# Kernel tuning notes

Hardware: AMD Instinct MI355X
Metric: run time of the kernel (lower is better)

Reference implementation:

```python
import jax, jax.numpy as jnp
import numpy as np
import math

# ---- physical constants (QMAV) ----
MASS = 1.5
GRAV = 9.81
_J_NP = np.diag([0.0211, 0.0219, 0.0366]).astype(np.float32)
J = jnp.asarray(_J_NP)
J_INV = jnp.asarray(np.linalg.inv(_J_NP).astype(np.float32))
KD_X = KD_Y = KD_Z = 0.10   # linear drag coeffs
K_H = 0.01                   # horizontal-velocity lift coeff
O_MIN, O_MAX = 0.0, 1000.0   # rotor speed limits [rad/s]
KT, KM, ARM = 1.0e-5, 1.0e-7, 0.15
_G_VEC = jnp.array([0.0, 0.0, GRAV], jnp.float32).reshape(1, 3, 1)  # NED, down positive


def make_G1():
    # [T, Mx, My, Mz] = G_1 @ [o1^2, o2^2, o3^2, o4^2], X-configuration mixer
    c = ARM * KT * math.sqrt(2.0) / 2.0
    return np.array([
        [KT,  KT,  KT,  KT],
        [-c,   c,   c,  -c],
        [-c,  -c,   c,   c],
        [-KM,  KM, -KM,  KM],
    ], dtype=np.float32)


def quat_to_rot(q):
    # q: [B,4,1] = (ew,ex,ey,ez) -> body-to-inertial rotation [B,3,3]
    ew, ex, ey, ez = q[:, 0, 0], q[:, 1, 0], q[:, 2, 0], q[:, 3, 0]
    r = jnp.stack([
        ew**2 + ex**2 - ey**2 - ez**2, 2*(ex*ey - ew*ez), 2*(ex*ez + ew*ey),
        2*(ex*ey + ew*ez), ew**2 - ex**2 + ey**2 - ez**2, 2*(ey*ez - ew*ex),
        2*(ex*ez - ew*ey), 2*(ey*ez + ew*ex), ew**2 - ex**2 - ey**2 + ez**2,
    ], axis=-1)
    return r.reshape(-1, 3, 3)


def quat_to_euler(q):
    ew, ex, ey, ez = q[:, 0:1, :], q[:, 1:2, :], q[:, 2:3, :], q[:, 3:4, :]
    phi = jnp.arctan2(2*(ew*ex + ey*ez), ew**2 + ez**2 - ex**2 - ey**2)
    theta = jnp.arcsin(jnp.clip(2*(ew*ey - ex*ez), -1.0, 1.0))
    psi = jnp.arctan2(2*(ew*ez + ex*ey), ew**2 + ex**2 - ey**2 - ez**2)
    return phi, theta, psi


def rigid_body_deriv(x, u):
    # x: [B,13,1] = [pos(3), v_world(3), quat(4), omega(3)]; u: [B,6,1] = [f_inertial(3), moment_body(3)]
    v = x[:, 3:6, :]
    q = x[:, 6:10, :]
    w = x[:, 10:13, :]
    f_i = u[:, 0:3, :]
    m_b = u[:, 3:6, :]
    pos_dot = v
    v_dot = f_i / MASS + _G_VEC
    ew, ex, ey, ez = q[:, 0:1, :], q[:, 1:2, :], q[:, 2:3, :], q[:, 3:4, :]
    p, qq, r = w[:, 0:1, :], w[:, 1:2, :], w[:, 2:3, :]
    q_dot = 0.5 * jnp.concatenate([
        -ex*p - ey*qq - ez*r,
         ew*p + ey*r - ez*qq,
         ew*qq - ex*r + ez*p,
         ew*r + ex*qq - ey*p,
    ], axis=1)
    Jw = jnp.einsum('ij,bjk->bik', J, w)
    w_dot = jnp.einsum('ij,bjk->bik', J_INV, m_b - jnp.cross(w, Jw, axis=1))
    return jnp.concatenate([pos_dot, v_dot, q_dot, w_dot], axis=1)


def rk4_step(x, u, dt):
    k1 = rigid_body_deriv(x, u)
    k2 = rigid_body_deriv(x + 0.5 * dt * k1, u)
    k3 = rigid_body_deriv(x + 0.5 * dt * k2, u)
    k4 = rigid_body_deriv(x + dt * k3, u)
    return x + (dt / 6.0) * (k1 + 2*k2 + 2*k3 + k4)


def setup_inputs() -> dict:
    key = jax.random.key(0)
    k1, k2 = jax.random.split(key)
    B = 1 << 20
    state = jax.random.normal(k1, (B, 32, 1), dtype=jnp.float32)
    # normalize the quaternion slice so the initial attitude is valid
    q = state[:, 9:13, :]
    state = state.at[:, 9:13, :].set(q / jnp.sqrt(jnp.sum(q**2, axis=1, keepdims=True)))
    delta = jax.random.uniform(k2, (B, 4, 1), dtype=jnp.float32) * O_MAX
    G_1 = jnp.asarray(make_G1())
    return {"state": state, "delta": delta, "G_1": G_1, "dt": 0.02}


def reference(state, delta, G_1, dt):
    # ---- forces / moments + wind-related state ----
    d = jnp.clip(delta, O_MIN, O_MAX)
    tt = jnp.einsum('ij,bjk->bik', G_1, d**2)  # [B,4,1] = [T, Mx, My, Mz]
    T = tt[:, 0:1, :]; Mx = tt[:, 1:2, :]; My = tt[:, 2:3, :]; Mz = tt[:, 3:4, :]
    R = quat_to_rot(state[:, 9:13, :])
    V_wind_b = jnp.einsum('bji,bjk->bik', R, state[:, 28:31, :])  # R^T @ wind_inertial
    u_r = state[:, 16:17, :] - V_wind_b[:, 0:1, :]
    v_r = state[:, 17:18, :] - V_wind_b[:, 1:2, :]
    w_r = state[:, 18:19, :] - V_wind_b[:, 2:3, :]
    Va = jnp.sqrt(u_r**2 + v_r**2 + w_r**2)
    u_safe = jnp.where(u_r == 0.0, 1.0, u_r)
    alpha = jnp.where(u_r == 0.0, math.pi / 2, jnp.arctan2(w_r, u_safe))
    Va_safe = jnp.where(Va == 0.0, 1.0, Va)
    beta = jnp.where(Va == 0.0, 0.0, jnp.arcsin(jnp.clip(v_r / Va_safe, -1.0, 1.0)))
    state = state.at[:, 22:23, :].set(Va)
    state = state.at[:, 24:25, :].set(alpha)
    state = state.at[:, 25:26, :].set(beta)
    fx = -KD_X * u_r
    fy = -KD_Y * v_r
    fz = -T - KD_Z * w_r + K_H * (u_r**2 + v_r**2)
    f_i = R @ jnp.concatenate([fx, fy, fz], axis=1)
    fm = jnp.concatenate([f_i, Mx, My, Mz], axis=1)  # [B,6,1]
    # ---- rigid-body RK4 integration ----
    ode_state = jnp.concatenate(
        [state[:, 3:6, :], state[:, 13:16, :], state[:, 9:13, :], state[:, 19:22, :]], axis=1)
    new = rk4_step(ode_state, fm, dt)
    qn = new[:, 6:10, :]
    qn = qn / jnp.sqrt(jnp.sum(qn**2, axis=1, keepdims=True))
    state = state.at[:, 3:6, :].set(new[:, 0:3, :])
    state = state.at[:, 13:16, :].set(new[:, 3:6, :])
    state = state.at[:, 9:13, :].set(qn)
    state = state.at[:, 19:22, :].set(new[:, 10:13, :])
    # ---- other derived states (R from the pre-update quaternion, as in original) ----
    phi, theta, psi = quat_to_euler(state[:, 9:13, :])
    pdot = R @ state[:, 16:19, :]
    Vg = jnp.sqrt(jnp.sum(pdot**2, axis=(1, 2)))[:, None, None]
    Vg_safe = jnp.where(Vg == 0.0, 1.0, Vg)
    gamma = jnp.arcsin(jnp.clip(pdot[:, 2:3, :] / Vg_safe, -1.0, 1.0))
    chi = jnp.arctan2(pdot[:, 1:2, :], pdot[:, 0:1, :])
    state = state.at[:, 6:7, :].set(phi)
    state = state.at[:, 7:8, :].set(theta)
    state = state.at[:, 8:9, :].set(psi)
    state = state.at[:, 23:24, :].set(Vg)
    state = state.at[:, 26:27, :].set(gamma)
    state = state.at[:, 27:28, :].set(chi)
    return state
```

## Files before the change

### kernel.cpp

```cpp
#include <hip/hip_runtime.h>
#include <math.h>


#define INV_MASSF  (1.0f / 1.5f)
#define GRAVF      9.81f
#define KDF        0.1f
#define KHF        0.01f
#define JXF        0.0211f
#define JYF        0.0219f
#define JZF        0.0366f
#define JIXF       (1.0f / 0.0211f)
#define JIYF       (1.0f / 0.0219f)
#define JIZF       (1.0f / 0.0366f)
#define PI_2F      1.57079632679489661923f

#define ROWS    256
#define STRIDE  36

__device__ __forceinline__ float clamp1(float x) {
    return fminf(fmaxf(x, -1.0f), 1.0f);
}

__device__ __forceinline__ void qw_deriv(const float x[7],
                                         float mx, float my, float mz,
                                         float k[7]) {
    const float ew = x[0], ex = x[1], ey = x[2], ez = x[3];
    const float p = x[4], q = x[5], r = x[6];
    k[0] = 0.5f * (-ex * p - ey * q - ez * r);
    k[1] = 0.5f * ( ew * p + ey * r - ez * q);
    k[2] = 0.5f * ( ew * q - ex * r + ez * p);
    k[3] = 0.5f * ( ew * r + ex * q - ey * p);
    const float Jwx = JXF * p, Jwy = JYF * q, Jwz = JZF * r;
    k[4] = (mx - (q * Jwz - r * Jwy)) * JIXF;
    k[5] = (my - (r * Jwx - p * Jwz)) * JIYF;
    k[6] = (mz - (p * Jwy - q * Jwx)) * JIZF;
}

__global__ __launch_bounds__(ROWS, 4) void qd_dynamics_kernel(
    const float* __restrict__ state,
    const float* __restrict__ delta,
    const float* __restrict__ G1,
    const float* __restrict__ dtp,
    float* __restrict__ out,
    int B)
{
    __shared__ float lds[ROWS * STRIDE];

    const int tid = threadIdx.x;
    const int row0 = blockIdx.x * ROWS;
    const bool full = (row0 + ROWS) <= B;

    const float dt = dtp[0];
    const float h2 = 0.5f * dt;

    float4 dl;
    if (full) {
        const float4* gp4 = (const float4*)(state + (size_t)row0 * 32);
        #pragma unroll
        for (int i = 0; i < 8; ++i) {
            const int f4 = i * ROWS + tid;
            const int r  = f4 >> 3;
            const int c4 = f4 & 7;
            *(float4*)&lds[r * STRIDE + c4 * 4] = gp4[f4];
        }
        dl = ((const float4*)delta)[row0 + tid];
    } else {
        const int last = B - 1;
        #pragma unroll
        for (int i = 0; i < 8; ++i) {
            const int f4 = i * ROWS + tid;
            const int r  = f4 >> 3;
            const int c4 = f4 & 7;
            const int gr = min(row0 + r, last);
            *(float4*)&lds[r * STRIDE + c4 * 4] =
                ((const float4*)state)[(size_t)gr * 8 + c4];
        }
        dl = ((const float4*)delta)[min(row0 + tid, last)];
    }
    __syncthreads();

    float T, Mx, My, Mz;
    {
        float d0 = fminf(fmaxf(dl.x, 0.0f), 1000.0f);
        float d1 = fminf(fmaxf(dl.y, 0.0f), 1000.0f);
        float d2 = fminf(fmaxf(dl.z, 0.0f), 1000.0f);
        float d3 = fminf(fmaxf(dl.w, 0.0f), 1000.0f);
        d0 *= d0; d1 *= d1; d2 *= d2; d3 *= d3;
        const float4* g4 = (const float4*)G1;
        const float4 g0 = g4[0], g1 = g4[1], g2 = g4[2], g3 = g4[3];
        T  = g0.x * d0 + g0.y * d1 + g0.z * d2 + g0.w * d3;
        Mx = g1.x * d0 + g1.y * d1 + g1.z * d2 + g1.w * d3;
        My = g2.x * d0 + g2.y * d1 + g2.z * d2 + g2.w * d3;
        Mz = g3.x * d0 + g3.y * d1 + g3.z * d2 + g3.w * d3;
    }

    float* row = &lds[tid * STRIDE];
    const float  pxo = row[3];
    const float2 pyz = *(const float2*)&row[4];
    const float4 A   = *(const float4*)&row[8];
    const float4 Bv  = *(const float4*)&row[12];
    const float4 C   = *(const float4*)&row[16];
    const float2 Dq  = *(const float2*)&row[20];
    const float4 Wd  = *(const float4*)&row[28];

    const float ew = A.y, ex = A.z, ey = A.w, ez = Bv.x;

    const float r00 = ew*ew + ex*ex - ey*ey - ez*ez;
    const float r01 = 2.0f * (ex*ey - ew*ez);
    const float r02 = 2.0f * (ex*ez + ew*ey);
    const float r10 = 2.0f * (ex*ey + ew*ez);
    const float r11 = ew*ew - ex*ex + ey*ey - ez*ez;
    const float r12 = 2.0f * (ey*ez - ew*ex);
    const float r20 = 2.0f * (ex*ez - ew*ey);
    const float r21 = 2.0f * (ey*ez + ew*ex);
    const float r22 = ew*ew - ex*ex - ey*ey + ez*ez;

    const float vwb0 = r00 * Wd.x + r10 * Wd.y + r20 * Wd.z;
    const float vwb1 = r01 * Wd.x + r11 * Wd.y + r21 * Wd.z;
    const float vwb2 = r02 * Wd.x + r12 * Wd.y + r22 * Wd.z;

    const float u_r = C.x - vwb0;
    const float v_r = C.y - vwb1;
    const float w_r = C.z - vwb2;
    const float Va = sqrtf(u_r * u_r + v_r * v_r + w_r * w_r);
    const float alpha = (u_r == 0.0f) ? PI_2F : atan2f(w_r, u_r);
    const float beta  = (Va == 0.0f) ? 0.0f : asinf(clamp1(v_r / Va));

    const float fx = -KDF * u_r;
    const float fy = -KDF * v_r;
    const float fz = -T - KDF * w_r + KHF * (u_r * u_r + v_r * v_r);
    const float vd0 = (r00 * fx + r01 * fy + r02 * fz) * INV_MASSF;
    const float vd1 = (r10 * fx + r11 * fy + r12 * fz) * INV_MASSF;
    const float vd2 = (r20 * fx + r21 * fy + r22 * fz) * INV_MASSF + GRAVF;

    const float vn0 = Bv.y + dt * vd0;
    const float vn1 = Bv.z + dt * vd1;
    const float vn2 = Bv.w + dt * vd2;
    const float hdt2 = 0.5f * dt * dt;
    const float pn0 = pxo   + dt * Bv.y + hdt2 * vd0;
    const float pn1 = pyz.x + dt * Bv.z + hdt2 * vd1;
    const float pn2 = pyz.y + dt * Bv.w + hdt2 * vd2;

    float x0[7] = {ew, ex, ey, ez, C.w, Dq.x, Dq.y};
    float k[7], acc[7], xt[7], xn[7];
    qw_deriv(x0, Mx, My, Mz, k);
    #pragma unroll
    for (int i = 0; i < 7; ++i) { acc[i] = k[i]; xt[i] = x0[i] + h2 * k[i]; }
    qw_deriv(xt, Mx, My, Mz, k);
    #pragma unroll
    for (int i = 0; i < 7; ++i) { acc[i] += 2.0f * k[i]; xt[i] = x0[i] + h2 * k[i]; }
    qw_deriv(xt, Mx, My, Mz, k);
    #pragma unroll
    for (int i = 0; i < 7; ++i) { acc[i] += 2.0f * k[i]; xt[i] = x0[i] + dt * k[i]; }
    qw_deriv(xt, Mx, My, Mz, k);
    const float dt6 = dt / 6.0f;
    #pragma unroll
    for (int i = 0; i < 7; ++i) xn[i] = x0[i] + dt6 * (acc[i] + k[i]);

    float qw2 = xn[0], qx2 = xn[1], qy2 = xn[2], qz2 = xn[3];
    const float qi = 1.0f / sqrtf(qw2*qw2 + qx2*qx2 + qy2*qy2 + qz2*qz2);
    qw2 *= qi; qx2 *= qi; qy2 *= qi; qz2 *= qi;

    const float phi = atan2f(2.0f * (qw2 * qx2 + qy2 * qz2),
                             qw2*qw2 + qz2*qz2 - qx2*qx2 - qy2*qy2);
    const float theta = asinf(clamp1(2.0f * (qw2 * qy2 - qx2 * qz2)));
    const float psi = atan2f(2.0f * (qw2 * qz2 + qx2 * qy2),
                             qw2*qw2 + qx2*qx2 - qy2*qy2 - qz2*qz2);

    const float p0 = r00 * C.x + r01 * C.y + r02 * C.z;
    const float p1 = r10 * C.x + r11 * C.y + r12 * C.z;
    const float p2 = r20 * C.x + r21 * C.y + r22 * C.z;
    const float Vg = sqrtf(p0 * p0 + p1 * p1 + p2 * p2);
    const float vgs = (Vg == 0.0f) ? 1.0f : Vg;
    const float gamma = asinf(clamp1(p2 / vgs));
    const float chi = atan2f(p1, p0);

    row[3] = pn0;
    *(float4*)&row[4]  = make_float4(pn1, pn2, phi, theta);
    *(float4*)&row[8]  = make_float4(psi, qw2, qx2, qy2);
    *(float4*)&row[12] = make_float4(qz2, vn0, vn1, vn2);
    row[19] = xn[4];
    *(float4*)&row[20] = make_float4(xn[5], xn[6], Va, Vg);
    *(float4*)&row[24] = make_float4(alpha, beta, gamma, chi);
    __syncthreads();

    if (full) {
        float4* op4 = (float4*)(out + (size_t)row0 * 32);
        #pragma unroll
        for (int i = 0; i < 8; ++i) {
            const int f4 = i * ROWS + tid;
            const int r  = f4 >> 3;
            const int c4 = f4 & 7;
            op4[f4] = *(const float4*)&lds[r * STRIDE + c4 * 4];
        }
    } else {
        #pragma unroll
        for (int i = 0; i < 8; ++i) {
            const int f4 = i * ROWS + tid;
            const int r  = f4 >> 3;
            const int c4 = f4 & 7;
            if (row0 + r < B)
                ((float4*)out)[(size_t)(row0 + r) * 8 + c4] =
                    *(const float4*)&lds[r * STRIDE + c4 * 4];
        }
    }
}

extern "C" void kernel_launch(void* const* d_in, const int* in_sizes, int n_in,
                              void* d_out, int out_size, void* d_ws, size_t ws_size,
                              hipStream_t stream) {
    const float* state = (const float*)d_in[0];
    const float* delta = (const float*)d_in[1];
    const float* G1    = (const float*)d_in[2];
    const float* dtp   = (const float*)d_in[3];
    float* out = (float*)d_out;
    const int B = in_sizes[0] / 32;
    const int grid = (B + ROWS - 1) / ROWS;
    hipLaunchKernelGGL(qd_dynamics_kernel, dim3(grid), dim3(ROWS), 0, stream,
                       state, delta, G1, dtp, out, B);
}
```

Baseline: 244.5 us.

## Stage state via direct global-to-LDS loads with XOR-swizzled layout

Replaces the register-staged global-to-LDS copy with the global_load_lds builtin, which writes 16-byte chunks straight into shared memory. It drops the padded stride-36 rows for a 32-float layout whose column chunks are XOR-swizzled by row to avoid bank conflicts. The compute is moved into a helper that reads and writes whole per-thread arrays, the tail block bypasses LDS, and the occupancy hint rises from 4 to 5 waves. The 16-byte direct-to-LDS load depends on gfx950 support, and the 32-float arrays per thread may raise register pressure.

```diff
diff --git a/kernel.cpp b/kernel.cpp
--- a/kernel.cpp
+++ b/kernel.cpp
@@ -15,7 +15,7 @@
 #define PI_2F      1.57079632679489661923f
 
 #define ROWS    256
-#define STRIDE  36
+#define RSTR    32
 
 __device__ __forceinline__ float clamp1(float x) {
     return fminf(fmaxf(x, -1.0f), 1.0f);
@@ -36,49 +36,9 @@
     k[6] = (mz - (p * Jwy - q * Jwx)) * JIZF;
 }
 
-__global__ __launch_bounds__(ROWS, 4) void qd_dynamics_kernel(
-    const float* __restrict__ state,
-    const float* __restrict__ delta,
-    const float* __restrict__ G1,
-    const float* __restrict__ dtp,
-    float* __restrict__ out,
-    int B)
-{
-    __shared__ float lds[ROWS * STRIDE];
-
-    const int tid = threadIdx.x;
-    const int row0 = blockIdx.x * ROWS;
-    const bool full = (row0 + ROWS) <= B;
-
-    const float dt = dtp[0];
-    const float h2 = 0.5f * dt;
-
-    float4 dl;
-    if (full) {
-        const float4* gp4 = (const float4*)(state + (size_t)row0 * 32);
-        #pragma unroll
-        for (int i = 0; i < 8; ++i) {
-            const int f4 = i * ROWS + tid;
-            const int r  = f4 >> 3;
-            const int c4 = f4 & 7;
-            *(float4*)&lds[r * STRIDE + c4 * 4] = gp4[f4];
-        }
-        dl = ((const float4*)delta)[row0 + tid];
-    } else {
-        const int last = B - 1;
-        #pragma unroll
-        for (int i = 0; i < 8; ++i) {
-            const int f4 = i * ROWS + tid;
-            const int r  = f4 >> 3;
-            const int c4 = f4 & 7;
-            const int gr = min(row0 + r, last);
-            *(float4*)&lds[r * STRIDE + c4 * 4] =
-                ((const float4*)state)[(size_t)gr * 8 + c4];
-        }
-        dl = ((const float4*)delta)[min(row0 + tid, last)];
-    }
-    __syncthreads();
-
+__device__ __forceinline__ void qd_compute(const float s[32], float4 dl,
+                                           const float* __restrict__ G1,
+                                           float dt, float o[32]) {
     float T, Mx, My, Mz;
     {
         float d0 = fminf(fmaxf(dl.x, 0.0f), 1000.0f);
@@ -94,16 +54,7 @@
         Mz = g3.x * d0 + g3.y * d1 + g3.z * d2 + g3.w * d3;
     }
 
-    float* row = &lds[tid * STRIDE];
-    const float  pxo = row[3];
-    const float2 pyz = *(const float2*)&row[4];
-    const float4 A   = *(const float4*)&row[8];
-    const float4 Bv  = *(const float4*)&row[12];
-    const float4 C   = *(const float4*)&row[16];
-    const float2 Dq  = *(const float2*)&row[20];
-    const float4 Wd  = *(const float4*)&row[28];
-
-    const float ew = A.y, ex = A.z, ey = A.w, ez = Bv.x;
+    const float ew = s[9], ex = s[10], ey = s[11], ez = s[12];
 
     const float r00 = ew*ew + ex*ex - ey*ey - ez*ez;
     const float r01 = 2.0f * (ex*ey - ew*ez);
@@ -115,13 +66,13 @@
     const float r21 = 2.0f * (ey*ez + ew*ex);
     const float r22 = ew*ew - ex*ex - ey*ey + ez*ez;
 
-    const float vwb0 = r00 * Wd.x + r10 * Wd.y + r20 * Wd.z;
-    const float vwb1 = r01 * Wd.x + r11 * Wd.y + r21 * Wd.z;
-    const float vwb2 = r02 * Wd.x + r12 * Wd.y + r22 * Wd.z;
-
-    const float u_r = C.x - vwb0;
-    const float v_r = C.y - vwb1;
-    const float w_r = C.z - vwb2;
+    const float vwb0 = r00 * s[28] + r10 * s[29] + r20 * s[30];
+    const float vwb1 = r01 * s[28] + r11 * s[29] + r21 * s[30];
+    const float vwb2 = r02 * s[28] + r12 * s[29] + r22 * s[30];
+
+    const float u_r = s[16] - vwb0;
+    const float v_r = s[17] - vwb1;
+    const float w_r = s[18] - vwb2;
     const float Va = sqrtf(u_r * u_r + v_r * v_r + w_r * w_r);
     const float alpha = (u_r == 0.0f) ? PI_2F : atan2f(w_r, u_r);
     const float beta  = (Va == 0.0f) ? 0.0f : asinf(clamp1(v_r / Va));
@@ -133,15 +84,16 @@
     const float vd1 = (r10 * fx + r11 * fy + r12 * fz) * INV_MASSF;
     const float vd2 = (r20 * fx + r21 * fy + r22 * fz) * INV_MASSF + GRAVF;
 
-    const float vn0 = Bv.y + dt * vd0;
-    const float vn1 = Bv.z + dt * vd1;
-    const float vn2 = Bv.w + dt * vd2;
+    const float vn0 = s[13] + dt * vd0;
+    const float vn1 = s[14] + dt * vd1;
+    const float vn2 = s[15] + dt * vd2;
     const float hdt2 = 0.5f * dt * dt;
-    const float pn0 = pxo   + dt * Bv.y + hdt2 * vd0;
-    const float pn1 = pyz.x + dt * Bv.z + hdt2 * vd1;
-    const float pn2 = pyz.y + dt * Bv.w + hdt2 * vd2;
-
-    float x0[7] = {ew, ex, ey, ez, C.w, Dq.x, Dq.y};
+    const float pn0 = s[3] + dt * s[13] + hdt2 * vd0;
+    const float pn1 = s[4] + dt * s[14] + hdt2 * vd1;
+    const float pn2 = s[5] + dt * s[15] + hdt2 * vd2;
+
+    const float h2 = 0.5f * dt;
+    float x0[7] = {ew, ex, ey, ez, s[19], s[20], s[21]};
     float k[7], acc[7], xt[7], xn[7];
     qw_deriv(x0, Mx, My, Mz, k);
     #pragma unroll
@@ -167,41 +119,99 @@
     const float psi = atan2f(2.0f * (qw2 * qz2 + qx2 * qy2),
                              qw2*qw2 + qx2*qx2 - qy2*qy2 - qz2*qz2);
 
-    const float p0 = r00 * C.x + r01 * C.y + r02 * C.z;
-    const float p1 = r10 * C.x + r11 * C.y + r12 * C.z;
-    const float p2 = r20 * C.x + r21 * C.y + r22 * C.z;
+    const float p0 = r00 * s[16] + r01 * s[17] + r02 * s[18];
+    const float p1 = r10 * s[16] + r11 * s[17] + r12 * s[18];
+    const float p2 = r20 * s[16] + r21 * s[17] + r22 * s[18];
     const float Vg = sqrtf(p0 * p0 + p1 * p1 + p2 * p2);
     const float vgs = (Vg == 0.0f) ? 1.0f : Vg;
     const float gamma = asinf(clamp1(p2 / vgs));
     const float chi = atan2f(p1, p0);
 
-    row[3] = pn0;
-    *(float4*)&row[4]  = make_float4(pn1, pn2, phi, theta);
-    *(float4*)&row[8]  = make_float4(psi, qw2, qx2, qy2);
-    *(float4*)&row[12] = make_float4(qz2, vn0, vn1, vn2);
-    row[19] = xn[4];
-    *(float4*)&row[20] = make_float4(xn[5], xn[6], Va, Vg);
-    *(float4*)&row[24] = make_float4(alpha, beta, gamma, chi);
-    __syncthreads();
+    o[0] = s[0]; o[1] = s[1]; o[2] = s[2];
+    o[3] = pn0; o[4] = pn1; o[5] = pn2;
+    o[6] = phi; o[7] = theta; o[8] = psi;
+    o[9] = qw2; o[10] = qx2; o[11] = qy2; o[12] = qz2;
+    o[13] = vn0; o[14] = vn1; o[15] = vn2;
+    o[16] = s[16]; o[17] = s[17]; o[18] = s[18];
+    o[19] = xn[4]; o[20] = xn[5]; o[21] = xn[6];
+    o[22] = Va; o[23] = Vg;
+    o[24] = alpha; o[25] = beta;
+    o[26] = gamma; o[27] = chi;
+    o[28] = s[28]; o[29] = s[29]; o[30] = s[30]; o[31] = s[31];
+}
+
+__global__ __launch_bounds__(ROWS, 5) void qd_dynamics_kernel(
+    const float* __restrict__ state,
+    const float* __restrict__ delta,
+    const float* __restrict__ G1,
+    const float* __restrict__ dtp,
+    float* __restrict__ out,
+    int B)
+{
+    __shared__ __align__(16) float lds[ROWS * RSTR];
+
+    const int tid = threadIdx.x;
+    const int row0 = blockIdx.x * ROWS;
+    const bool full = (row0 + ROWS) <= B;
+
+    const float dt = dtp[0];
+
+    float s[32], o[32];
+    float4 dl;
 
     if (full) {
-        float4* op4 = (float4*)(out + (size_t)row0 * 32);
+        const float* gbase = state + (size_t)row0 * 32;
         #pragma unroll
         for (int i = 0; i < 8; ++i) {
             const int f4 = i * ROWS + tid;
             const int r  = f4 >> 3;
             const int c4 = f4 & 7;
-            op4[f4] = *(const float4*)&lds[r * STRIDE + c4 * 4];
+            const int sc = c4 ^ (r & 7);
+            __builtin_amdgcn_global_load_lds(
+                (const __attribute__((address_space(1))) void*)
+                    (gbase + (size_t)r * 32 + sc * 4),
+                (__attribute__((address_space(3))) void*)(&lds[f4 * 4]),
+                16, 0, 0);
         }
+        dl = ((const float4*)delta)[row0 + tid];
+        __syncthreads();
+
+        #pragma unroll
+        for (int lc = 0; lc < 8; ++lc)
+            ((float4*)s)[lc] =
+                *(const float4*)&lds[(tid * 8 + (lc ^ (tid & 7))) * 4];
     } else {
+        const int b = row0 + tid;
+        const int bb = (b < B) ? b : (B - 1);
+        const float4* sp = (const float4*)(state + (size_t)bb * 32);
+        #pragma unroll
+        for (int i = 0; i < 8; ++i) ((float4*)s)[i] = sp[i];
+        dl = ((const float4*)delta)[bb];
+    }
+
+    qd_compute(s, dl, G1, dt, o);
+
+    if (full) {
+        #pragma unroll
+        for (int lc = 0; lc < 8; ++lc)
+            *(float4*)&lds[(tid * 8 + (lc ^ (tid & 7))) * 4] =
+                ((const float4*)o)[lc];
+        __syncthreads();
+        float4* op4 = (float4*)(out + (size_t)row0 * 32);
         #pragma unroll
         for (int i = 0; i < 8; ++i) {
             const int f4 = i * ROWS + tid;
             const int r  = f4 >> 3;
             const int c4 = f4 & 7;
-            if (row0 + r < B)
-                ((float4*)out)[(size_t)(row0 + r) * 8 + c4] =
-                    *(const float4*)&lds[r * STRIDE + c4 * 4];
+            const int sc = c4 ^ (r & 7);
+            op4[(size_t)r * 8 + sc] = *(const float4*)&lds[f4 * 4];
+        }
+    } else {
+        const int b = row0 + tid;
+        if (b < B) {
+            float4* op = (float4*)(out + (size_t)b * 32);
+            #pragma unroll
+            for (int i = 0; i < 8; ++i) op[i] = ((const float4*)o)[i];
         }
     }
 }
```

Result: slower. 252.9 us (+3.4%).
